# Optimization experiments

Measured on AMD Instinct MI355X. Metric: run time of the kernel, lower is better.

## Reference

```python
import jax, jax.numpy as jnp
import numpy as np

DIM = 1024
NUM_HEADS = 16
HEAD_DIM = DIM // NUM_HEADS
SCALE = HEAD_DIM ** (-0.5)


def setup_inputs() -> dict:
    key = jax.random.key(0)
    ks = jax.random.split(key, 5)
    B, N, C = 2, 2048, DIM
    q = jax.random.normal(ks[0], (B, N, C), dtype=jnp.float32)
    k = jax.random.normal(ks[1], (B, N, C), dtype=jnp.float32)
    v = jax.random.normal(ks[2], (B, N, C), dtype=jnp.float32)
    # fused qkv Linear weight, torch layout [3*C, C]; no bias (qkv_bias=False)
    qkv_w = jax.random.normal(ks[3], (3 * C, C), dtype=jnp.float32) * (C ** -0.5)
    proj_w = jax.random.normal(ks[4], (C, C), dtype=jnp.float32) * (C ** -0.5)
    proj_b = jnp.zeros((C,), dtype=jnp.float32)
    return {"q": q, "k": k, "v": v, "qkv_w": qkv_w, "proj_w": proj_w,
            "proj_b": proj_b, "use_mask": 1}


def reference(q, k, v, qkv_w, proj_w, proj_b, use_mask):
    B, N, C = q.shape
    N_k = k.shape[1]
    H, hd = NUM_HEADS, HEAD_DIM
    # The original applies the full fused qkv Linear to each of q,k,v and keeps
    # only slice 0/1/2 respectively; computing just the used slice is identical math.
    wq, wk, wv = qkv_w[:C], qkv_w[C:2 * C], qkv_w[2 * C:]
    qh = (q @ wq.T).reshape(B, N, H, hd).transpose(0, 2, 1, 3)      # [B,H,N,hd]
    kh = (k @ wk.T).reshape(B, N_k, H, hd).transpose(0, 2, 1, 3)    # [B,H,Nk,hd]
    vh = (v @ wv.T).reshape(B, N_k, H, hd).transpose(0, 2, 1, 3)    # [B,H,Nk,hd]
    attn = jnp.einsum('bhnd,bhmd->bhnm', qh, kh) * SCALE            # [B,H,N,Nk]
    if use_mask:  # static Python flag -> causal tril mask as in the source
        msk = jnp.tril(jnp.ones((N, N_k), dtype=bool))
        attn = jnp.where(msk[None, None], attn, jnp.float32(-1e9))
    attn = jax.nn.softmax(attn, axis=-1)
    x = jnp.einsum('bhnm,bhmd->bhnd', attn, vh)                     # [B,H,N,hd]
    x = x.transpose(0, 2, 1, 3).reshape(B, N, C)
    x = x @ proj_w.T + proj_b
    return x, attn
```

## Files before the change

kernel.cpp:

```cpp
#include <hip/hip_runtime.h>


typedef unsigned short u16;
typedef unsigned int u32;
typedef __attribute__((ext_vector_type(8))) short s16x8;
typedef __attribute__((ext_vector_type(4))) float f32x4;
typedef __attribute__((ext_vector_type(4))) u16 u16x4;

#define AS1 __attribute__((address_space(1)))
#define AS3 __attribute__((address_space(3)))

static __device__ __forceinline__ u16 f2bf(float f) {
  u32 u = __builtin_bit_cast(u32, f);
  u = (u + 0x7fffu + ((u >> 16) & 1u)) >> 16;
  return (u16)u;
}

static __device__ __forceinline__ void gll16(const u16* g, u16* l) {
  __builtin_amdgcn_global_load_lds((const AS1 u32*)g, (AS3 u32*)l, 16, 0, 0);
}

static __device__ __forceinline__ f32x4 mfma_bf16(s16x8 a, s16x8 b, f32x4 c) {
  return __builtin_amdgcn_mfma_f32_16x16x32_bf16(a, b, c, 0, 0, 0);
}

__global__ __launch_bounds__(256) void cast_kernel(const float* __restrict__ in,
                                                   u16* __restrict__ out, int n4) {
  int i = blockIdx.x * 256 + threadIdx.x;
  if (i < n4) {
    f32x4 v = ((const f32x4*)in)[i];
    u16x4 o = { f2bf(v.x), f2bf(v.y), f2bf(v.z), f2bf(v.w) };
    ((u16x4*)out)[i] = o;
  }
}

static __device__ __forceinline__ void gemm_core_1024(
    const u16* __restrict__ A, const u16* __restrict__ Bm,
    int m0, int n0, int t, u16* a_s, u16* b_s, f32x4 acc[4][4]) {
  const int lane = t & 63;
  const int w = t >> 6;
  const int wm = (w & 1) * 64, wn = (w >> 1) * 64;
  const int lrow = lane & 15, lq = lane >> 4;
  const int r0 = t >> 2;
  const int c0 = (t & 3) * 8;

  for (int kt = 0; kt < 1024; kt += 32) {
    __syncthreads();
    gll16(A  + (size_t)(m0 + r0)      * 1024 + kt + c0, &a_s[(size_t)t * 8]);
    gll16(A  + (size_t)(m0 + r0 + 64) * 1024 + kt + c0, &a_s[(size_t)(t + 256) * 8]);
    gll16(Bm + (size_t)(n0 + r0)      * 1024 + kt + c0, &b_s[(size_t)t * 8]);
    gll16(Bm + (size_t)(n0 + r0 + 64) * 1024 + kt + c0, &b_s[(size_t)(t + 256) * 8]);
    __syncthreads();
    s16x8 af[4], bfr[4];
#pragma unroll
    for (int x = 0; x < 4; x++) af[x]  = *(const s16x8*)&a_s[(wm + x*16 + lrow)*32 + lq*8];
#pragma unroll
    for (int x = 0; x < 4; x++) bfr[x] = *(const s16x8*)&b_s[(wn + x*16 + lrow)*32 + lq*8];
#pragma unroll
    for (int tm = 0; tm < 4; tm++)
#pragma unroll
      for (int tn = 0; tn < 4; tn++)
        acc[tm][tn] = mfma_bf16(af[tm], bfr[tn], acc[tm][tn]);
  }
}

__global__ __launch_bounds__(256) void gemm_qkv_kernel(
    const u16* __restrict__ qb, const u16* __restrict__ kb, const u16* __restrict__ vb,
    const u16* __restrict__ wb, u16* __restrict__ Qh, u16* __restrict__ Kh,
    u16* __restrict__ Vt) {
  __shared__ u16 a_s[128*32], b_s[128*32];
  const int mode = blockIdx.z;
  const u16* A = (mode == 0) ? qb : (mode == 1) ? kb : vb;
  const u16* Bm = wb + (size_t)mode * (1024 * 1024);
  const int m0 = blockIdx.y * 128, n0 = blockIdx.x * 128;
  const int t = threadIdx.x;
  f32x4 acc[4][4];
  const f32x4 Z = {0.f, 0.f, 0.f, 0.f};
#pragma unroll
  for (int i = 0; i < 4; i++)
#pragma unroll
    for (int j = 0; j < 4; j++) acc[i][j] = Z;

  gemm_core_1024(A, Bm, m0, n0, t, a_s, b_s, acc);

  const int lane = t & 63, w = t >> 6;
  const int wm = (w & 1) * 64, wn = (w >> 1) * 64;
  const int lrow = lane & 15, lq = lane >> 4;
#pragma unroll
  for (int tm = 0; tm < 4; tm++) {
#pragma unroll
    for (int tn = 0; tn < 4; tn++) {
      const int ng = n0 + wn + tn * 16 + lrow;
      const int h = ng >> 6, d = ng & 63;
#pragma unroll
      for (int i = 0; i < 4; i++) {
        const int mg = m0 + wm + tm * 16 + lq * 4 + i;
        const int b = mg >> 11, s = mg & 2047;
        const float v = acc[tm][tn][i];
        if (mode == 0)
          Qh[((size_t)(b * 16 + h) * 2048 + s) * 64 + d] = f2bf(v * 0.125f);
        else if (mode == 1)
          Kh[((size_t)(b * 16 + h) * 2048 + s) * 64 + d] = f2bf(v);
        else
          Vt[((size_t)(b * 16 + h) * 64 + d) * 2048 + s] = f2bf(v);
      }
    }
  }
}

__global__ __launch_bounds__(256) void gemm_proj_kernel(
    const u16* __restrict__ xatt, const u16* __restrict__ pwb,
    const float* __restrict__ bias, float* __restrict__ out) {
  __shared__ u16 a_s[128*32], b_s[128*32];
  const int m0 = blockIdx.y * 128, n0 = blockIdx.x * 128;
  const int t = threadIdx.x;
  f32x4 acc[4][4];
  const f32x4 Z = {0.f, 0.f, 0.f, 0.f};
#pragma unroll
  for (int i = 0; i < 4; i++)
#pragma unroll
    for (int j = 0; j < 4; j++) acc[i][j] = Z;

  gemm_core_1024(xatt, pwb, m0, n0, t, a_s, b_s, acc);

  const int lane = t & 63, w = t >> 6;
  const int wm = (w & 1) * 64, wn = (w >> 1) * 64;
  const int lrow = lane & 15, lq = lane >> 4;
#pragma unroll
  for (int tn = 0; tn < 4; tn++) {
    const int ng = n0 + wn + tn * 16 + lrow;
    const float bv = bias[ng];
#pragma unroll
    for (int tm = 0; tm < 4; tm++) {
#pragma unroll
      for (int i = 0; i < 4; i++) {
        const int mg = m0 + wm + tm * 16 + lq * 4 + i;
        out[(size_t)mg * 1024 + ng] = acc[tm][tn][i] + bv;
      }
    }
  }
}


static __device__ __forceinline__ void qk_tile(const s16x8 qf[2], const s16x8 kf[4][2],
                                               f32x4 sacc[4]) {
  const f32x4 Z = {0.f, 0.f, 0.f, 0.f};
#pragma unroll
  for (int tn = 0; tn < 4; tn++) {
    sacc[tn] = Z;
#pragma unroll
    for (int kq = 0; kq < 2; kq++)
      sacc[tn] = mfma_bf16(qf[kq], kf[tn][kq], sacc[tn]);
  }
}

static __device__ __forceinline__ void expsum_tile(const f32x4 sacc[4], bool diag,
                                                   int lrow, int rbase, float l_acc[4]) {
  float part[4] = {0.f, 0.f, 0.f, 0.f};
#pragma unroll
  for (int tn = 0; tn < 4; tn++)
#pragma unroll
    for (int i = 0; i < 4; i++) {
      const bool ok = !diag || (tn * 16 + lrow <= rbase + i);
      part[i] += ok ? __expf(sacc[tn][i]) : 0.f;
    }
#pragma unroll
  for (int i = 0; i < 4; i++) {
    float s = part[i];
    s += __shfl_xor(s, 1, 16);
    s += __shfl_xor(s, 2, 16);
    s += __shfl_xor(s, 4, 16);
    s += __shfl_xor(s, 8, 16);
    l_acc[i] += s;
  }
}

static __device__ __forceinline__ void p_tile(const f32x4 sacc[4], bool diag, int lrow,
                                              int lq, int w, const float inv_l[4],
                                              float* __restrict__ abase, u16* p_w,
                                              s16x8 pf[2]) {
#pragma unroll
  for (int tn = 0; tn < 4; tn++)
#pragma unroll
    for (int i = 0; i < 4; i++) {
      const int rl = lq * 4 + i;
      const bool ok = !diag || (tn * 16 + lrow <= w * 16 + rl);
      const float pv = ok ? __expf(sacc[tn][i]) * inv_l[i] : 0.f;
      abase[(size_t)rl * 2048 + tn * 16 + lrow] = pv;
      p_w[rl * 72 + tn * 16 + lrow] = f2bf(pv);
    }
#pragma unroll
  for (int kq = 0; kq < 2; kq++)
    pf[kq] = *(const s16x8*)&p_w[lrow * 72 + kq * 32 + lq * 8];
}

__global__ __launch_bounds__(256) void attn_kernel(
    const u16* __restrict__ Qh, const u16* __restrict__ Kh, const u16* __restrict__ Vt,
    float* __restrict__ attn, u16* __restrict__ xatt, const int* __restrict__ use_mask_p) {
  __shared__ u16 smem[8192 + 8192 + 8 * 16 * 72];
  u16* k_s = smem;
  u16* vq  = smem + 8192;
  u16* p_s = smem + 16384;

  const int bh = blockIdx.y;
  const int p  = blockIdx.x;
  const int t = threadIdx.x;
  const int lane = t & 63, w = t >> 6;
  const int lrow = lane & 15, lq = lane >> 4;
  const int use_mask = *use_mask_p;

  const int q0[2] = { p * 64, (31 - p) * 64 };
  const int Tc[2] = { use_mask ? p : 31, use_mask ? 31 - p : 31 };
  const int Tmax  = Tc[1];

  const int rs  = t >> 3;
  const int csw = (((t & 7) ^ (rs & 7)) * 8);
  const int sk  = (lrow & 7) << 3;

  const u16* kg = Kh + (size_t)bh * (2048 * 64);
  const u16* vg = Vt + (size_t)bh * (64 * 2048);

  {
    const u16* qgA = Qh + ((size_t)bh * 2048 + q0[0]) * 64;
    const u16* qgB = Qh + ((size_t)bh * 2048 + q0[1]) * 64;
    gll16(qgA + (size_t)rs * 64 + csw,        &vq[t * 8]);
    gll16(qgA + (size_t)(rs + 32) * 64 + csw, &vq[(t + 256) * 8]);
    gll16(qgB + (size_t)rs * 64 + csw,        &vq[4096 + t * 8]);
    gll16(qgB + (size_t)(rs + 32) * 64 + csw, &vq[4096 + (t + 256) * 8]);
    gll16(kg + (size_t)rs * 64 + csw,         &k_s[t * 8]);
    gll16(kg + (size_t)(rs + 32) * 64 + csw,  &k_s[(t + 256) * 8]);
  }
  __syncthreads();

  s16x8 qf[2][2];
  const int qrow = w * 16 + lrow;
#pragma unroll
  for (int kq = 0; kq < 2; kq++) {
    qf[0][kq] = *(const s16x8*)&vq[qrow * 64 + ((kq * 32 + lq * 8) ^ sk)];
    qf[1][kq] = *(const s16x8*)&vq[4096 + qrow * 64 + ((kq * 32 + lq * 8) ^ sk)];
  }

  const int rbase = w * 16 + lq * 4;

  float l_acc[2][4];
#pragma unroll
  for (int c = 0; c < 2; c++)
#pragma unroll
    for (int i = 0; i < 4; i++) l_acc[c][i] = 0.f;

  for (int tt = 0; tt <= Tmax; tt++) {
    const int cur = tt & 1;
    if (tt < Tmax) {
      gll16(kg + (size_t)((tt + 1) * 64 + rs) * 64 + csw,      &k_s[(cur ^ 1) * 4096 + t * 8]);
      gll16(kg + (size_t)((tt + 1) * 64 + rs + 32) * 64 + csw, &k_s[(cur ^ 1) * 4096 + (t + 256) * 8]);
    }
    s16x8 kf[4][2];
#pragma unroll
    for (int tn = 0; tn < 4; tn++)
#pragma unroll
      for (int kq = 0; kq < 2; kq++)
        kf[tn][kq] = *(const s16x8*)&k_s[cur * 4096 + (tn * 16 + lrow) * 64 + ((kq * 32 + lq * 8) ^ sk)];
    f32x4 sacc[4];
    __builtin_amdgcn_s_setprio(1);
    qk_tile(qf[1], kf, sacc);
    __builtin_amdgcn_s_setprio(0);
    expsum_tile(sacc, use_mask && (tt == Tc[1]), lrow, rbase, l_acc[1]);
    if (tt <= Tc[0]) {
      __builtin_amdgcn_s_setprio(1);
      qk_tile(qf[0], kf, sacc);
      __builtin_amdgcn_s_setprio(0);
      expsum_tile(sacc, use_mask && (tt == Tc[0]), lrow, rbase, l_acc[0]);
    }
    __syncthreads();
  }

  float inv_l[2][4];
#pragma unroll
  for (int c = 0; c < 2; c++)
#pragma unroll
    for (int i = 0; i < 4; i++) inv_l[c][i] = 1.0f / l_acc[c][i];

  f32x4 oacc[2][4];
  const f32x4 Z = {0.f, 0.f, 0.f, 0.f};
#pragma unroll
  for (int c = 0; c < 2; c++)
#pragma unroll
    for (int i = 0; i < 4; i++) oacc[c][i] = Z;

  gll16(kg + (size_t)rs * 64 + csw,          &k_s[t * 8]);
  gll16(kg + (size_t)(rs + 32) * 64 + csw,   &k_s[(t + 256) * 8]);
  gll16(vg + (size_t)rs * 2048 + csw,        &vq[t * 8]);
  gll16(vg + (size_t)(rs + 32) * 2048 + csw, &vq[(t + 256) * 8]);
  __syncthreads();

  for (int tt = 0; tt <= Tmax; tt++) {
    const int cur = tt & 1;
    if (tt < Tmax) {
      gll16(kg + (size_t)((tt + 1) * 64 + rs) * 64 + csw,        &k_s[(cur ^ 1) * 4096 + t * 8]);
      gll16(kg + (size_t)((tt + 1) * 64 + rs + 32) * 64 + csw,   &k_s[(cur ^ 1) * 4096 + (t + 256) * 8]);
      gll16(vg + (size_t)rs * 2048 + (tt + 1) * 64 + csw,        &vq[(cur ^ 1) * 4096 + t * 8]);
      gll16(vg + (size_t)(rs + 32) * 2048 + (tt + 1) * 64 + csw, &vq[(cur ^ 1) * 4096 + (t + 256) * 8]);
    }
    const bool act0 = (tt <= Tc[0]);
    s16x8 kf[4][2];
#pragma unroll
    for (int tn = 0; tn < 4; tn++)
#pragma unroll
      for (int kq = 0; kq < 2; kq++)
        kf[tn][kq] = *(const s16x8*)&k_s[cur * 4096 + (tn * 16 + lrow) * 64 + ((kq * 32 + lq * 8) ^ sk)];

    f32x4 sacc1[4], sacc0[4];
    __builtin_amdgcn_s_setprio(1);
    qk_tile(qf[1], kf, sacc1);
    if (act0) qk_tile(qf[0], kf, sacc0);
    __builtin_amdgcn_s_setprio(0);

    s16x8 pf1[2], pf0[2];
    {
      float* abase = attn + ((size_t)(bh * 2048 + q0[1] + w * 16)) * 2048 + tt * 64;
      p_tile(sacc1, use_mask && (tt == Tc[1]), lrow, lq, w, inv_l[1], abase,
             p_s + (w * 2 + 1) * 1152, pf1);
    }
    if (act0) {
      float* abase = attn + ((size_t)(bh * 2048 + q0[0] + w * 16)) * 2048 + tt * 64;
      p_tile(sacc0, use_mask && (tt == Tc[0]), lrow, lq, w, inv_l[0], abase,
             p_s + (w * 2 + 0) * 1152, pf0);
    }

    s16x8 vf[4][2];
#pragma unroll
    for (int td = 0; td < 4; td++)
#pragma unroll
      for (int kq = 0; kq < 2; kq++)
        vf[td][kq] = *(const s16x8*)&vq[cur * 4096 + (td * 16 + lrow) * 64 + ((kq * 32 + lq * 8) ^ sk)];

    __builtin_amdgcn_s_setprio(1);
#pragma unroll
    for (int td = 0; td < 4; td++)
#pragma unroll
      for (int kq = 0; kq < 2; kq++)
        oacc[1][td] = mfma_bf16(pf1[kq], vf[td][kq], oacc[1][td]);
    if (act0) {
#pragma unroll
      for (int td = 0; td < 4; td++)
#pragma unroll
        for (int kq = 0; kq < 2; kq++)
          oacc[0][td] = mfma_bf16(pf0[kq], vf[td][kq], oacc[0][td]);
    }
    __builtin_amdgcn_s_setprio(0);
    __syncthreads();
  }

  const int b = bh >> 4, h = bh & 15;
#pragma unroll
  for (int c = 0; c < 2; c++)
#pragma unroll
    for (int td = 0; td < 4; td++)
#pragma unroll
      for (int i = 0; i < 4; i++) {
        const int row = q0[c] + w * 16 + lq * 4 + i;
        xatt[((size_t)(b * 2048 + row)) * 1024 + h * 64 + td * 16 + lrow] = f2bf(oacc[c][td][i]);
      }

  if (use_mask) {
    const f32x4 Z4 = {0.f, 0.f, 0.f, 0.f};
#pragma unroll
    for (int c = 0; c < 2; c++) {
      const int zc0 = q0[c] + 64;
      if (zc0 < 2048) {
        const int nzv = (2048 - zc0) >> 2;
        f32x4* zb = (f32x4*)(attn + ((size_t)bh * 2048 + q0[c]) * 2048 + zc0);
        const int row = t >> 2;
        for (int cc = (t & 3); cc < nzv; cc += 4)
          zb[(size_t)row * 512 + cc] = Z4;
      }
    }
  }
}

extern "C" void kernel_launch(void* const* d_in, const int* in_sizes, int n_in,
                              void* d_out, int out_size, void* d_ws, size_t ws_size,
                              hipStream_t stream) {
  const float* q      = (const float*)d_in[0];
  const float* k      = (const float*)d_in[1];
  const float* v      = (const float*)d_in[2];
  const float* qkv_w  = (const float*)d_in[3];
  const float* proj_w = (const float*)d_in[4];
  const float* proj_b = (const float*)d_in[5];
  const int*   use_mask = (const int*)d_in[6];

  const size_t MB = 1024 * 1024;
  char* ws = (char*)d_ws;
  u16* qb  = (u16*)(ws + 0 * MB);
  u16* kb  = (u16*)(ws + 8 * MB);
  u16* vb  = (u16*)(ws + 16 * MB);
  u16* wb  = (u16*)(ws + 24 * MB);
  u16* pwb = (u16*)(ws + 30 * MB);
  u16* Qh  = (u16*)(ws + 32 * MB);
  u16* Kh  = (u16*)(ws + 40 * MB);
  u16* Vt  = (u16*)(ws + 48 * MB);
  u16* xat = qb;

  float* out_x    = (float*)d_out;
  float* out_attn = out_x + (size_t)2 * 2048 * 1024;

  cast_kernel<<<4096, 256, 0, stream>>>(q, qb, 1048576);
  cast_kernel<<<4096, 256, 0, stream>>>(k, kb, 1048576);
  cast_kernel<<<4096, 256, 0, stream>>>(v, vb, 1048576);
  cast_kernel<<<3072, 256, 0, stream>>>(qkv_w, wb, 786432);
  cast_kernel<<<1024, 256, 0, stream>>>(proj_w, pwb, 262144);

  gemm_qkv_kernel<<<dim3(8, 32, 3), 256, 0, stream>>>(qb, kb, vb, wb, Qh, Kh, Vt);
  attn_kernel<<<dim3(16, 32), 256, 0, stream>>>(Qh, Kh, Vt, out_attn, xat, use_mask);
  gemm_proj_kernel<<<dim3(8, 32), 256, 0, stream>>>(xat, pwb, proj_b, out_x);
}
```

Measured before the change: 729.9 us.

## Stage attention probabilities through LDS for coalesced stores and fuse cast kernels

```diff
diff --git a/kernel.cpp b/kernel.cpp
--- a/kernel.cpp
+++ b/kernel.cpp
@@ -24,14 +24,22 @@
   return __builtin_amdgcn_mfma_f32_16x16x32_bf16(a, b, c, 0, 0, 0);
 }
 
-__global__ __launch_bounds__(256) void cast_kernel(const float* __restrict__ in,
-                                                   u16* __restrict__ out, int n4) {
+__global__ __launch_bounds__(256) void cast_all_kernel(
+    const float* __restrict__ q, const float* __restrict__ k, const float* __restrict__ v,
+    const float* __restrict__ qkv_w, const float* __restrict__ proj_w,
+    u16* __restrict__ qb, u16* __restrict__ kb, u16* __restrict__ vb,
+    u16* __restrict__ wb, u16* __restrict__ pwb) {
   int i = blockIdx.x * 256 + threadIdx.x;
-  if (i < n4) {
-    f32x4 v = ((const f32x4*)in)[i];
-    u16x4 o = { f2bf(v.x), f2bf(v.y), f2bf(v.z), f2bf(v.w) };
-    ((u16x4*)out)[i] = o;
-  }
+  const float* src; u16* dst; int off;
+  if (i < 1048576)       { src = q;      dst = qb;  off = i; }
+  else if (i < 2097152)  { src = k;      dst = kb;  off = i - 1048576; }
+  else if (i < 3145728)  { src = v;      dst = vb;  off = i - 2097152; }
+  else if (i < 3932160)  { src = qkv_w;  dst = wb;  off = i - 3145728; }
+  else if (i < 4194304)  { src = proj_w; dst = pwb; off = i - 3932160; }
+  else return;
+  f32x4 vv = ((const f32x4*)src)[off];
+  u16x4 o = { f2bf(vv.x), f2bf(vv.y), f2bf(vv.z), f2bf(vv.w) };
+  ((u16x4*)dst)[off] = o;
 }
 
 static __device__ __forceinline__ void gemm_core_1024(
@@ -175,32 +183,47 @@
   }
 }
 
-static __device__ __forceinline__ void p_tile(const f32x4 sacc[4], bool diag, int lrow,
-                                              int lq, int w, const float inv_l[4],
-                                              float* __restrict__ abase, u16* p_w,
-                                              s16x8 pf[2]) {
+static __device__ __forceinline__ void p_phase(const f32x4 sacc[4], bool diag,
+                                               int lane, int lrow, int lq, int w,
+                                               const float invl[4], float* pw,
+                                               float* __restrict__ gb, s16x8 pf[2]) {
 #pragma unroll
   for (int tn = 0; tn < 4; tn++)
 #pragma unroll
     for (int i = 0; i < 4; i++) {
       const int rl = lq * 4 + i;
       const bool ok = !diag || (tn * 16 + lrow <= w * 16 + rl);
-      const float pv = ok ? __expf(sacc[tn][i]) * inv_l[i] : 0.f;
-      abase[(size_t)rl * 2048 + tn * 16 + lrow] = pv;
-      p_w[rl * 72 + tn * 16 + lrow] = f2bf(pv);
-    }
-#pragma unroll
-  for (int kq = 0; kq < 2; kq++)
-    pf[kq] = *(const s16x8*)&p_w[lrow * 72 + kq * 32 + lq * 8];
-}
-
-__global__ __launch_bounds__(256) void attn_kernel(
+      const float pv = ok ? __expf(sacc[tn][i]) * invl[i] : 0.f;
+      pw[rl * 68 + tn * 16 + lrow] = pv;
+    }
+  const int rr = lane >> 3, c8 = (lane & 7) * 4;
+#pragma unroll
+  for (int j = 0; j < 2; j++)
+#pragma unroll
+    for (int m = 0; m < 2; m++) {
+      f32x4 vv = *(const f32x4*)&pw[(rr + 8 * j) * 68 + m * 32 + c8];
+      *(f32x4*)&gb[(size_t)(rr + 8 * j) * 2048 + m * 32 + c8] = vv;
+    }
+#pragma unroll
+  for (int kq = 0; kq < 2; kq++) {
+    f32x4 lo = *(const f32x4*)&pw[lrow * 68 + kq * 32 + lq * 8];
+    f32x4 hi = *(const f32x4*)&pw[lrow * 68 + kq * 32 + lq * 8 + 4];
+    s16x8 r;
+    r[0] = (short)f2bf(lo.x); r[1] = (short)f2bf(lo.y);
+    r[2] = (short)f2bf(lo.z); r[3] = (short)f2bf(lo.w);
+    r[4] = (short)f2bf(hi.x); r[5] = (short)f2bf(hi.y);
+    r[6] = (short)f2bf(hi.z); r[7] = (short)f2bf(hi.w);
+    pf[kq] = r;
+  }
+}
+
+__global__ __launch_bounds__(256, 2) void attn_kernel(
     const u16* __restrict__ Qh, const u16* __restrict__ Kh, const u16* __restrict__ Vt,
     float* __restrict__ attn, u16* __restrict__ xatt, const int* __restrict__ use_mask_p) {
-  __shared__ u16 smem[8192 + 8192 + 8 * 16 * 72];
+  __shared__ u16 smem[8192 + 8192];
+  __shared__ float p32[4][16 * 68];
   u16* k_s = smem;
   u16* vq  = smem + 8192;
-  u16* p_s = smem + 16384;
 
   const int bh = blockIdx.y;
   const int p  = blockIdx.x;
@@ -293,6 +316,8 @@
   gll16(vg + (size_t)(rs + 32) * 2048 + csw, &vq[(t + 256) * 8]);
   __syncthreads();
 
+  float* pw = &p32[w][0];
+
   for (int tt = 0; tt <= Tmax; tt++) {
     const int cur = tt & 1;
     if (tt < Tmax) {
@@ -308,25 +333,6 @@
 #pragma unroll
       for (int kq = 0; kq < 2; kq++)
         kf[tn][kq] = *(const s16x8*)&k_s[cur * 4096 + (tn * 16 + lrow) * 64 + ((kq * 32 + lq * 8) ^ sk)];
-
-    f32x4 sacc1[4], sacc0[4];
-    __builtin_amdgcn_s_setprio(1);
-    qk_tile(qf[1], kf, sacc1);
-    if (act0) qk_tile(qf[0], kf, sacc0);
-    __builtin_amdgcn_s_setprio(0);
-
-    s16x8 pf1[2], pf0[2];
-    {
-      float* abase = attn + ((size_t)(bh * 2048 + q0[1] + w * 16)) * 2048 + tt * 64;
-      p_tile(sacc1, use_mask && (tt == Tc[1]), lrow, lq, w, inv_l[1], abase,
-             p_s + (w * 2 + 1) * 1152, pf1);
-    }
-    if (act0) {
-      float* abase = attn + ((size_t)(bh * 2048 + q0[0] + w * 16)) * 2048 + tt * 64;
-      p_tile(sacc0, use_mask && (tt == Tc[0]), lrow, lq, w, inv_l[0], abase,
-             p_s + (w * 2 + 0) * 1152, pf0);
-    }
-
     s16x8 vf[4][2];
 #pragma unroll
     for (int td = 0; td < 4; td++)
@@ -334,20 +340,38 @@
       for (int kq = 0; kq < 2; kq++)
         vf[td][kq] = *(const s16x8*)&vq[cur * 4096 + (td * 16 + lrow) * 64 + ((kq * 32 + lq * 8) ^ sk)];
 
-    __builtin_amdgcn_s_setprio(1);
-#pragma unroll
-    for (int td = 0; td < 4; td++)
-#pragma unroll
-      for (int kq = 0; kq < 2; kq++)
-        oacc[1][td] = mfma_bf16(pf1[kq], vf[td][kq], oacc[1][td]);
+    {
+      f32x4 sacc[4];
+      __builtin_amdgcn_s_setprio(1);
+      qk_tile(qf[1], kf, sacc);
+      __builtin_amdgcn_s_setprio(0);
+      s16x8 pf[2];
+      float* gb = attn + ((size_t)(bh * 2048 + q0[1] + w * 16)) * 2048 + tt * 64;
+      p_phase(sacc, use_mask && (tt == Tc[1]), lane, lrow, lq, w, inv_l[1], pw, gb, pf);
+      __builtin_amdgcn_s_setprio(1);
+#pragma unroll
+      for (int td = 0; td < 4; td++)
+#pragma unroll
+        for (int kq = 0; kq < 2; kq++)
+          oacc[1][td] = mfma_bf16(pf[kq], vf[td][kq], oacc[1][td]);
+      __builtin_amdgcn_s_setprio(0);
+    }
     if (act0) {
+      f32x4 sacc[4];
+      __builtin_amdgcn_s_setprio(1);
+      qk_tile(qf[0], kf, sacc);
+      __builtin_amdgcn_s_setprio(0);
+      s16x8 pf[2];
+      float* gb = attn + ((size_t)(bh * 2048 + q0[0] + w * 16)) * 2048 + tt * 64;
+      p_phase(sacc, use_mask && (tt == Tc[0]), lane, lrow, lq, w, inv_l[0], pw, gb, pf);
+      __builtin_amdgcn_s_setprio(1);
 #pragma unroll
       for (int td = 0; td < 4; td++)
 #pragma unroll
         for (int kq = 0; kq < 2; kq++)
-          oacc[0][td] = mfma_bf16(pf0[kq], vf[td][kq], oacc[0][td]);
-    }
-    __builtin_amdgcn_s_setprio(0);
+          oacc[0][td] = mfma_bf16(pf[kq], vf[td][kq], oacc[0][td]);
+      __builtin_amdgcn_s_setprio(0);
+    }
     __syncthreads();
   }
 
@@ -364,15 +388,18 @@
 
   if (use_mask) {
     const f32x4 Z4 = {0.f, 0.f, 0.f, 0.f};
+    const int rr = t >> 3;
+    const int c8 = (t & 7) * 4;
 #pragma unroll
     for (int c = 0; c < 2; c++) {
       const int zc0 = q0[c] + 64;
       if (zc0 < 2048) {
-        const int nzv = (2048 - zc0) >> 2;
-        f32x4* zb = (f32x4*)(attn + ((size_t)bh * 2048 + q0[c]) * 2048 + zc0);
-        const int row = t >> 2;
-        for (int cc = (t & 3); cc < nzv; cc += 4)
-          zb[(size_t)row * 512 + cc] = Z4;
+        const int n32 = (2048 - zc0) >> 5;
+        float* zb = attn + ((size_t)bh * 2048 + q0[c]) * 2048 + zc0;
+        for (int j = 0; j < n32; j++) {
+          *(f32x4*)&zb[(size_t)rr * 2048 + j * 32 + c8] = Z4;
+          *(f32x4*)&zb[(size_t)(rr + 32) * 2048 + j * 32 + c8] = Z4;
+        }
       }
     }
   }
@@ -404,11 +431,7 @@
   float* out_x    = (float*)d_out;
   float* out_attn = out_x + (size_t)2 * 2048 * 1024;
 
-  cast_kernel<<<4096, 256, 0, stream>>>(q, qb, 1048576);
-  cast_kernel<<<4096, 256, 0, stream>>>(k, kb, 1048576);
-  cast_kernel<<<4096, 256, 0, stream>>>(v, vb, 1048576);
-  cast_kernel<<<3072, 256, 0, stream>>>(qkv_w, wb, 786432);
-  cast_kernel<<<1024, 256, 0, stream>>>(proj_w, pwb, 262144);
+  cast_all_kernel<<<16384, 256, 0, stream>>>(q, k, v, qkv_w, proj_w, qb, kb, vb, wb, pwb);
 
   gemm_qkv_kernel<<<dim3(8, 32, 3), 256, 0, stream>>>(qb, kb, vb, wb, Qh, Kh, Vt);
   attn_kernel<<<dim3(16, 32), 256, 0, stream>>>(Qh, Kh, Vt, out_attn, xat, use_mask);
```

After: 715.2 us. 1.02x faster.
